# Kernel optimization log

Hardware: AMD Instinct MI355X
Metric: run time of the kernel (lower is better)

## Reference

```python
import jax, jax.numpy as jnp
import numpy as np

B, S, H = 1, 2048, 4096
NH = 32
HD = H // NH  # 128
HALF = HD // 2
BASE = 10000.0


def setup_inputs() -> dict:
    key = jax.random.key(0)
    k1, k2, k3 = jax.random.split(key, 3)
    hidden_states = jax.random.normal(k1, (B, S, H), dtype=jnp.float32)
    W_qkv = jax.random.normal(k2, (H, 3 * H), dtype=jnp.float32) * 0.02
    W_o = jax.random.normal(k3, (H, H), dtype=jnp.float32) * 0.02
    # causal additive mask [B,1,S,S]: 0 on/below diagonal, large negative above
    causal = jnp.triu(jnp.full((S, S), -1e9, dtype=jnp.float32), k=1)
    attention_mask = jnp.broadcast_to(causal[None, None], (B, 1, S, S))
    position_ids = jnp.broadcast_to(jnp.arange(S, dtype=jnp.int64)[None, :], (B, S))
    return {
        'hidden_states': hidden_states,
        'W_qkv': W_qkv,
        'W_o': W_o,
        'attention_mask': attention_mask,
        'position_ids': position_ids,
    }


def _rope(x, cos, sin):
    # x: [b,s,nh,hd]; cos/sin: [b,s,1,half]. Half-split rotation as in the Triton kernel.
    x1, x2 = x[..., :HALF], x[..., HALF:]
    return jnp.concatenate([x1 * cos - x2 * sin, x1 * sin + x2 * cos], axis=-1)


def reference(hidden_states, W_qkv, W_o, attention_mask, position_ids):
    b, s, h = hidden_states.shape
    # fused QKV projection (dequantized GPTQ matmul == dense matmul math)
    qkv = jnp.einsum('bsh,hk->bsk', hidden_states, W_qkv).reshape(b, s, 3, NH, HD)
    # RoPE angles: freq = exp(col * INV_BASE) * position_id, INV_BASE = -2 ln(base)/head_dim
    inv_base = -2.0 * np.log(BASE) / HD
    freqs = jnp.exp(jnp.arange(HALF, dtype=jnp.float32) * inv_base)  # [half]
    theta = position_ids.astype(jnp.float32)[:, :, None] * freqs      # [b,s,half]
    cos = jnp.cos(theta)[:, :, None, :]
    sin = jnp.sin(theta)[:, :, None, :]
    q = _rope(qkv[:, :, 0], cos, sin).transpose(0, 2, 1, 3)  # [b,nh,s,hd]
    k = _rope(qkv[:, :, 1], cos, sin).transpose(0, 2, 1, 3)
    v = qkv[:, :, 2].transpose(0, 2, 1, 3)
    scores = jnp.einsum('bhqd,bhkd->bhqk', q, k) / np.sqrt(HD).astype(np.float32)
    scores = scores + attention_mask
    scores = jnp.maximum(scores, jnp.finfo(scores.dtype).min)
    attn = jax.nn.softmax(scores.astype(jnp.float32), axis=-1).astype(q.dtype)
    out = jnp.einsum('bhqk,bhkd->bqhd', attn, v).reshape(b, s, h)
    return jnp.einsum('bsh,ho->bso', out, W_o)
```

## Files before the change

kernel.cpp:

```cpp
#include <hip/hip_runtime.h>

#define S_LEN 2048
#define HDIM 4096
#define NHEADS 32
#define HEAD_DIM 128
#define HALF_DIM 64
#define N_QKV 12288
#define QK_COLS 8192

typedef __attribute__((ext_vector_type(8))) short short8;
typedef __attribute__((ext_vector_type(4))) float f32x4;

typedef const __attribute__((address_space(1))) unsigned int gu32;
typedef __attribute__((address_space(3))) unsigned int lu32;

__device__ __forceinline__ void gload_lds16(const void* g, void* l) {
    __builtin_amdgcn_global_load_lds((gu32*)g, (lu32*)l, 16, 0, 0);
}

__device__ __forceinline__ unsigned short f2bf(float f) {
    unsigned int u = __float_as_uint(f);
    u += 0x7fff + ((u >> 16) & 1);
    return (unsigned short)(u >> 16);
}

__device__ __forceinline__ void xcd_map(int& bx, int& by) {
    int gx = gridDim.x;
    int lin = blockIdx.y * gx + blockIdx.x;
    int x = lin & 7, c = lin >> 3;
    int bxp = gx >> 3;
    bx = bxp * x + c % bxp;
    by = c / bxp;
}


__global__ __launch_bounds__(256) void cvt_hs_k(const float* __restrict__ in,
                                                unsigned short* __restrict__ out, int n4) {
    int i = blockIdx.x * 256 + threadIdx.x;
    if (i >= n4) return;
    float4 v = reinterpret_cast<const float4*>(in)[i];
    ushort4 o;
    o.x = f2bf(v.x); o.y = f2bf(v.y); o.z = f2bf(v.z); o.w = f2bf(v.w);
    reinterpret_cast<ushort4*>(out)[i] = o;
}

__device__ __forceinline__ int permute_col(int n) {
    if (n < QK_COLS) {
        int hd = n & 127;
        int base = n - hd;
        int e = hd & 63;
        int d2 = (e & 15) + 32 * (e >> 4) + ((hd >> 6) << 4);
        return base + d2;
    }
    return n;
}

template <bool PERM>
__global__ __launch_bounds__(256) void tconv_k(const float* __restrict__ in,
                                               unsigned short* __restrict__ out, int R, int C) {
    __shared__ float tile[64][65];
    int c0 = blockIdx.x * 64, r0 = blockIdx.y * 64;
    int tx = threadIdx.x & 63, ty = threadIdx.x >> 6;
#pragma unroll
    for (int i = 0; i < 16; ++i) {
        int r = ty + i * 4;
        tile[r][tx] = in[(size_t)(r0 + r) * C + c0 + tx];
    }
    __syncthreads();
#pragma unroll
    for (int i = 0; i < 16; ++i) {
        int c = ty + i * 4;
        int n = PERM ? permute_col(c0 + c) : (c0 + c);
        out[(size_t)n * R + r0 + tx] = f2bf(tile[tx][c]);
    }
}

__global__ __launch_bounds__(256) void rope_tab_k(const int* __restrict__ pos_raw,
                                                  float* __restrict__ ctab,
                                                  float* __restrict__ stab) {
    int i = blockIdx.x * 256 + threadIdx.x;
    int s = i >> 6, d = i & 63;
    bool is64 = (pos_raw[1] == 0 && pos_raw[2] == 1);
    int p = is64 ? pos_raw[2 * s] : pos_raw[s];
    const float INVB = -0.14391156831212787f;
    float freq = expf((float)d * INVB);
    float th = (float)p * freq;
    ctab[i] = cosf(th);
    stab[i] = sinf(th);
}


__device__ __forceinline__ void mainloop(const unsigned short* __restrict__ Ag,
                                         const unsigned short* __restrict__ Bg,
                                         int K, int m0, int n0,
                                         char* As, char* Bs,
                                         f32x4 (&acc)[4][4]) {
    const int tid = threadIdx.x;
    const int wid = tid >> 6, lane = tid & 63, l15 = lane & 15, l4 = lane >> 4;
    const int wm = wid >> 1, wn = wid & 1;
    const int NT = K >> 6;

    size_t abase[4], bbase[4];
    int off[4];
#pragma unroll
    for (int i = 0; i < 4; ++i) {
        int p = (i * 256 + tid) << 4;
        int q = p ^ (((p >> 7) & 7) << 4);
        abase[i] = (size_t)(m0 + (q >> 7)) * K + ((q & 127) >> 1);
        bbase[i] = (size_t)(n0 + (q >> 7)) * K + ((q & 127) >> 1);
        off[i] = p;
    }

    for (int t = 0; t < NT; ++t) {
        int k0 = t << 6;
#pragma unroll
        for (int i = 0; i < 4; ++i) gload_lds16(Ag + abase[i] + k0, As + off[i]);
#pragma unroll
        for (int i = 0; i < 4; ++i) gload_lds16(Bg + bbase[i] + k0, Bs + off[i]);
        asm volatile("s_waitcnt vmcnt(0)" ::: "memory");
        __builtin_amdgcn_s_barrier();

        short8 a[4][2], b[4][2];
#pragma unroll
        for (int am = 0; am < 4; ++am)
#pragma unroll
            for (int ks = 0; ks < 2; ++ks) {
                int lin = ((wm * 64 + am * 16 + l15) << 7) + ks * 64 + l4 * 16;
                a[am][ks] = *(const short8*)(As + (lin ^ (((lin >> 7) & 7) << 4)));
            }
#pragma unroll
        for (int bn = 0; bn < 4; ++bn)
#pragma unroll
            for (int ks = 0; ks < 2; ++ks) {
                int lin = ((wn * 64 + bn * 16 + l15) << 7) + ks * 64 + l4 * 16;
                b[bn][ks] = *(const short8*)(Bs + (lin ^ (((lin >> 7) & 7) << 4)));
            }
#pragma unroll
        for (int ks = 0; ks < 2; ++ks)
#pragma unroll
            for (int am = 0; am < 4; ++am)
#pragma unroll
                for (int bn = 0; bn < 4; ++bn)
                    acc[am][bn] = __builtin_amdgcn_mfma_f32_16x16x32_bf16(a[am][ks], b[bn][ks], acc[am][bn], 0, 0, 0);

        __builtin_amdgcn_s_barrier();
    }
}

__global__ __launch_bounds__(256, 3) void gemm1_k(const unsigned short* __restrict__ A,
                                                  const unsigned short* __restrict__ Bt,
                                                  const float* __restrict__ ctab,
                                                  const float* __restrict__ stab,
                                                  unsigned short* __restrict__ qb,
                                                  unsigned short* __restrict__ kb,
                                                  unsigned short* __restrict__ vt) {
    __shared__ __attribute__((aligned(16))) char As[16384];
    __shared__ __attribute__((aligned(16))) char Bs[16384];

    int bx, by;
    xcd_map(bx, by);
    int m0 = by * 128, n0 = bx * 128;

    f32x4 acc[4][4];
#pragma unroll
    for (int i = 0; i < 4; ++i)
#pragma unroll
        for (int j = 0; j < 4; ++j) acc[i][j] = (f32x4){0.f, 0.f, 0.f, 0.f};

    mainloop(A, Bt, HDIM, m0, n0, As, Bs, acc);

    int tid = threadIdx.x, wid = tid >> 6, lane = tid & 63, l15 = lane & 15, l4 = lane >> 4;
    int wm = wid >> 1, wn = wid & 1;
    int which = n0 >> 12;
    int head = (n0 & 4095) >> 7;
    if (which < 2) {
        unsigned short* dst = which ? kb : qb;
#pragma unroll
        for (int am = 0; am < 4; ++am)
#pragma unroll
            for (int j = 0; j < 4; ++j) {
                int s = m0 + wm * 64 + am * 16 + l4 * 4 + j;
#pragma unroll
                for (int p = 0; p < 2; ++p) {
                    float x1 = acc[am][2 * p][j], x2 = acc[am][2 * p + 1][j];
                    int e = l15 + 16 * (2 * wn + p);
                    float cs = ctab[s * 64 + e], sn = stab[s * 64 + e];
                    dst[((size_t)head * S_LEN + s) * HEAD_DIM + e] = f2bf(x1 * cs - x2 * sn);
                    dst[((size_t)head * S_LEN + s) * HEAD_DIM + e + 64] = f2bf(x1 * sn + x2 * cs);
                }
            }
    } else {
#pragma unroll
        for (int am = 0; am < 4; ++am)
#pragma unroll
            for (int j = 0; j < 4; ++j) {
                int s = m0 + wm * 64 + am * 16 + l4 * 4 + j;
#pragma unroll
                for (int bn = 0; bn < 4; ++bn) {
                    int d = wn * 64 + bn * 16 + l15;
                    vt[((size_t)head * HEAD_DIM + d) * S_LEN + s] = f2bf(acc[am][bn][j]);
                }
            }
    }
}

__global__ __launch_bounds__(256, 3) void gemm2_k(const unsigned short* __restrict__ A,
                                                  const unsigned short* __restrict__ Bt,
                                                  float* __restrict__ out) {
    __shared__ __attribute__((aligned(16))) char As[16384];
    __shared__ __attribute__((aligned(16))) char Bs[16384];

    int bx, by;
    xcd_map(bx, by);
    int m0 = by * 128, n0 = bx * 128;

    f32x4 acc[4][4];
#pragma unroll
    for (int i = 0; i < 4; ++i)
#pragma unroll
        for (int j = 0; j < 4; ++j) acc[i][j] = (f32x4){0.f, 0.f, 0.f, 0.f};

    mainloop(A, Bt, HDIM, m0, n0, As, Bs, acc);

    int tid = threadIdx.x, wid = tid >> 6, lane = tid & 63, l15 = lane & 15, l4 = lane >> 4;
    int wm = wid >> 1, wn = wid & 1;
#pragma unroll
    for (int am = 0; am < 4; ++am)
#pragma unroll
        for (int j = 0; j < 4; ++j) {
            int s = m0 + wm * 64 + am * 16 + l4 * 4 + j;
#pragma unroll
            for (int bn = 0; bn < 4; ++bn)
                out[(size_t)s * HDIM + n0 + wn * 64 + bn * 16 + l15] = acc[am][bn][j];
        }
}

__global__ __launch_bounds__(256) void flash_k(const unsigned short* __restrict__ Q,
                                               const unsigned short* __restrict__ Kb,
                                               const unsigned short* __restrict__ Vt,
                                               float* __restrict__ O_parts,
                                               float* __restrict__ ml) {
    __shared__ __attribute__((aligned(16))) char Ks[2][16384];
    __shared__ __attribute__((aligned(16))) char Vs[2][16384];
    __shared__ __attribute__((aligned(16))) char Ps[4][4096];
    int h = blockIdx.y;
    int bx2 = 39 - (int)blockIdx.x;
    int qblk, spl;
    if (bx2 < 4)       { qblk = bx2;                 spl = 0; }
    else if (bx2 < 12) { qblk = 4 + ((bx2 - 4) >> 1);  spl = (bx2 - 4) & 1; }
    else if (bx2 < 24) { int u = bx2 - 12; int q3 = u / 3; qblk = 8 + q3; spl = u - 3 * q3; }
    else               { qblk = 12 + ((bx2 - 24) >> 2); spl = (bx2 - 24) & 3; }
    int pidx = h * 40 + bx2;
    int kv_start = spl << 9;
    int kv_end = min((qblk + 1) << 7, (spl + 1) << 9);
    int NT = (kv_end - kv_start) >> 6;

    int tid = threadIdx.x, w = tid >> 6, lane = tid & 63, l15 = lane & 15, l4 = lane >> 4;
    int qrow0 = qblk * 128 + w * 32;

    const unsigned short* Kg = Kb + (size_t)h * S_LEN * HEAD_DIM;
    const unsigned short* Vg = Vt + (size_t)h * HEAD_DIM * S_LEN;

    short8 qf[2][4];
#pragma unroll
    for (int mt = 0; mt < 2; ++mt) {
        int s = qrow0 + mt * 16 + l15;
#pragma unroll
        for (int ks = 0; ks < 4; ++ks)
            qf[mt][ks] = *(const short8*)(Q + ((size_t)h * S_LEN + s) * HEAD_DIM + ks * 32 + l4 * 8);
    }

    float m_run[2][4];
    f32x4 o[2][8];
    f32x4 lsum[2];
#pragma unroll
    for (int mt = 0; mt < 2; ++mt) {
#pragma unroll
        for (int j = 0; j < 4; ++j) m_run[mt][j] = -1e30f;
        lsum[mt] = (f32x4){0.f, 0.f, 0.f, 0.f};
#pragma unroll
        for (int dt = 0; dt < 8; ++dt) o[mt][dt] = (f32x4){0.f, 0.f, 0.f, 0.f};
    }

    int lofs[4];
    size_t kgofs[4], vgofs[4];
#pragma unroll
    for (int i = 0; i < 4; ++i) {
        int p = (i * 256 + tid) << 4;
        lofs[i] = p;
        int qk = p ^ (((p >> 8) & 7) << 4);
        kgofs[i] = (size_t)(qk >> 8) * HEAD_DIM + ((qk & 255) >> 1);
        int qv = p ^ (((p >> 7) & 7) << 4);
        vgofs[i] = (size_t)(qv >> 7) * S_LEN + ((qv & 127) >> 1);
    }

    auto stage = [&](int t) {
        char* Kd = Ks[t & 1];
        char* Vd = Vs[t & 1];
        size_t kvoff = (size_t)(kv_start + t * 64);
#pragma unroll
        for (int i = 0; i < 4; ++i) gload_lds16(Kg + kvoff * HEAD_DIM + kgofs[i], Kd + lofs[i]);
#pragma unroll
        for (int i = 0; i < 4; ++i) gload_lds16(Vg + kvoff + vgofs[i], Vd + lofs[i]);
    };

    const float scale = 0.08838834764831845f;

    short8 onesv;
#pragma unroll
    for (int e = 0; e < 8; ++e) onesv[e] = (short)0x3F80;

    stage(0);

    for (int t = 0; t < NT; ++t) {
        int cur = t & 1;
        if (t + 1 < NT) {
            stage(t + 1);
            asm volatile("s_waitcnt vmcnt(8)" ::: "memory");
        } else {
            asm volatile("s_waitcnt vmcnt(0)" ::: "memory");
        }
        __builtin_amdgcn_sched_barrier(0);
        __builtin_amdgcn_s_barrier();
        __builtin_amdgcn_sched_barrier(0);

        f32x4 sc[2][4];
#pragma unroll
        for (int mt = 0; mt < 2; ++mt)
#pragma unroll
            for (int nt = 0; nt < 4; ++nt) sc[mt][nt] = (f32x4){0.f, 0.f, 0.f, 0.f};
#pragma unroll
        for (int ks = 0; ks < 4; ++ks) {
            short8 kfr[4];
#pragma unroll
            for (int nt = 0; nt < 4; ++nt) {
                int lin = ((nt * 16 + l15) << 8) + ks * 64 + l4 * 16;
                kfr[nt] = *(const short8*)(Ks[cur] + (lin ^ (((lin >> 8) & 7) << 4)));
            }
#pragma unroll
            for (int mt = 0; mt < 2; ++mt)
#pragma unroll
                for (int nt = 0; nt < 4; ++nt)
                    sc[mt][nt] = __builtin_amdgcn_mfma_f32_16x16x32_bf16(qf[mt][ks], kfr[nt], sc[mt][nt], 0, 0, 0);
        }

        float pmax[2][4];
        bool need = false;
#pragma unroll
        for (int mt = 0; mt < 2; ++mt)
#pragma unroll
            for (int j = 0; j < 4; ++j) {
                int srow = qrow0 + mt * 16 + l4 * 4 + j;
                int c = kv_start + t * 64 + l15;
                float v0 = (c      <= srow) ? sc[mt][0][j] * scale : -1e30f;
                float v1 = (c + 16 <= srow) ? sc[mt][1][j] * scale : -1e30f;
                float v2 = (c + 32 <= srow) ? sc[mt][2][j] * scale : -1e30f;
                float v3 = (c + 48 <= srow) ? sc[mt][3][j] * scale : -1e30f;
                sc[mt][0][j] = v0; sc[mt][1][j] = v1; sc[mt][2][j] = v2; sc[mt][3][j] = v3;
                float mx = fmaxf(fmaxf(v0, v1), fmaxf(v2, v3));
                mx = fmaxf(mx, __shfl_xor(mx, 1));
                mx = fmaxf(mx, __shfl_xor(mx, 2));
                mx = fmaxf(mx, __shfl_xor(mx, 4));
                mx = fmaxf(mx, __shfl_xor(mx, 8));
                pmax[mt][j] = mx;
                need = need || (mx > m_run[mt][j] + 8.0f);
            }
        if (__any(need ? 1 : 0)) {
#pragma unroll
            for (int mt = 0; mt < 2; ++mt)
#pragma unroll
                for (int j = 0; j < 4; ++j) {
                    float mnew = fmaxf(m_run[mt][j], pmax[mt][j]);
                    float r = __expf(m_run[mt][j] - mnew);
                    m_run[mt][j] = mnew;
                    lsum[mt][j] *= r;
#pragma unroll
                    for (int dt = 0; dt < 8; ++dt) o[mt][dt][j] *= r;
                }
        }

#pragma unroll
        for (int mt = 0; mt < 2; ++mt)
#pragma unroll
            for (int j = 0; j < 4; ++j) {
                int prow = mt * 16 + l4 * 4 + j;
                int rb = prow << 7;
                int sw = (prow & 7) << 4;
#pragma unroll
                for (int nt = 0; nt < 4; ++nt) {
                    unsigned short pb = f2bf(__expf(sc[mt][nt][j] - m_run[mt][j]));
                    *(unsigned short*)(Ps[w] + ((rb + (l15 + nt * 16) * 2) ^ sw)) = pb;
                }
            }
        asm volatile("s_waitcnt lgkmcnt(0)" ::: "memory");
        __builtin_amdgcn_sched_barrier(0);

        short8 pf[2][2];
#pragma unroll
        for (int mt = 0; mt < 2; ++mt)
#pragma unroll
            for (int k2 = 0; k2 < 2; ++k2) {
                int lin = ((mt * 16 + l15) << 7) + k2 * 64 + l4 * 16;
                pf[mt][k2] = *(const short8*)(Ps[w] + (lin ^ (((lin >> 7) & 7) << 4)));
            }
#pragma unroll
        for (int k2 = 0; k2 < 2; ++k2)
#pragma unroll
            for (int mt = 0; mt < 2; ++mt)
                lsum[mt] = __builtin_amdgcn_mfma_f32_16x16x32_bf16(pf[mt][k2], onesv, lsum[mt], 0, 0, 0);
#pragma unroll
        for (int dt = 0; dt < 8; ++dt) {
#pragma unroll
            for (int k2 = 0; k2 < 2; ++k2) {
                int lin = ((dt * 16 + l15) << 7) + k2 * 64 + l4 * 16;
                short8 vf = *(const short8*)(Vs[cur] + (lin ^ (((lin >> 7) & 7) << 4)));
#pragma unroll
                for (int mt = 0; mt < 2; ++mt)
                    o[mt][dt] = __builtin_amdgcn_mfma_f32_16x16x32_bf16(pf[mt][k2], vf, o[mt][dt], 0, 0, 0);
            }
        }
        __builtin_amdgcn_sched_barrier(0);
        __builtin_amdgcn_s_barrier();
        __builtin_amdgcn_sched_barrier(0);
    }

    float* Op = O_parts + (size_t)pidx * 16384;
#pragma unroll
    for (int mt = 0; mt < 2; ++mt)
#pragma unroll
        for (int j = 0; j < 4; ++j) {
            int rloc = w * 32 + mt * 16 + l4 * 4 + j;
#pragma unroll
            for (int dt = 0; dt < 8; ++dt)
                Op[rloc * 128 + dt * 16 + l15] = o[mt][dt][j];
            if (l15 == 0) {
                ml[(size_t)pidx * 256 + rloc] = m_run[mt][j];
                ml[(size_t)pidx * 256 + 128 + rloc] = lsum[mt][j];
            }
        }
}

__global__ __launch_bounds__(256) void reduce_k(const float* __restrict__ Op,
                                                const float* __restrict__ ml,
                                                unsigned short* __restrict__ ctx) {
    int qblk = blockIdx.x, h = blockIdx.y;
    int ns = (qblk >> 2) + 1;
    int st;
    if (qblk < 4) st = qblk;
    else if (qblk < 8) st = 4 + 2 * (qblk - 4);
    else if (qblk < 12) st = 12 + 3 * (qblk - 8);
    else st = 24 + 4 * (qblk - 12);
    int p0 = h * 40 + st;
#pragma unroll
    for (int it = 0; it < 16; ++it) {
        int idx = it * 256 + threadIdx.x;
        int row = idx >> 5, dq = idx & 31;
        float mstar = -1e30f;
        for (int s = 0; s < ns; ++s)
            mstar = fmaxf(mstar, ml[(size_t)(p0 + s) * 256 + row]);
        f32x4 acc = (f32x4){0.f, 0.f, 0.f, 0.f};
        float lt = 0.f;
        for (int s = 0; s < ns; ++s) {
            float wgt = __expf(ml[(size_t)(p0 + s) * 256 + row] - mstar);
            lt += wgt * ml[(size_t)(p0 + s) * 256 + 128 + row];
            f32x4 ov = *(const f32x4*)(Op + (size_t)(p0 + s) * 16384 + row * 128 + dq * 4);
            acc += ov * wgt;
        }
        float inv = 1.0f / lt;
        int grow = qblk * 128 + row;
        ushort4 o4;
        o4.x = f2bf(acc[0] * inv);
        o4.y = f2bf(acc[1] * inv);
        o4.z = f2bf(acc[2] * inv);
        o4.w = f2bf(acc[3] * inv);
        *(ushort4*)(ctx + (size_t)grow * HDIM + h * 128 + dq * 4) = o4;
    }
}


extern "C" void kernel_launch(void* const* d_in, const int* in_sizes, int n_in,
                              void* d_out, int out_size, void* d_ws, size_t ws_size,
                              hipStream_t stream) {
    const float* hs = (const float*)d_in[0];
    const float* wqkv = (const float*)d_in[1];
    const float* wo = (const float*)d_in[2];
    const int* pos = (const int*)d_in[4];
    float* out = (float*)d_out;
    char* ws = (char*)d_ws;
    const size_t MB = 1024 * 1024;

    unsigned short* hs_b = (unsigned short*)(ws);
    unsigned short* wq_t = (unsigned short*)(ws + 16 * MB);
    unsigned short* wo_t = (unsigned short*)(ws + 112 * MB);
    unsigned short* qbuf = (unsigned short*)(ws + 144 * MB);
    unsigned short* kbuf = (unsigned short*)(ws + 160 * MB);
    unsigned short* vtb  = (unsigned short*)(ws + 176 * MB);
    unsigned short* ctx  = (unsigned short*)(ws + 192 * MB);
    float* ctab = (float*)(ws + 208 * MB);
    float* stab = (float*)(ws + 209 * MB);
    float* O_parts = (float*)(ws + 16 * MB);
    float* ml_buf  = (float*)(ws + 96 * MB);

    cvt_hs_k<<<(S_LEN * HDIM / 4 + 255) / 256, 256, 0, stream>>>(hs, hs_b, S_LEN * HDIM / 4);
    tconv_k<true><<<dim3(N_QKV / 64, HDIM / 64), 256, 0, stream>>>(wqkv, wq_t, HDIM, N_QKV);
    tconv_k<false><<<dim3(HDIM / 64, HDIM / 64), 256, 0, stream>>>(wo, wo_t, HDIM, HDIM);
    rope_tab_k<<<(S_LEN * 64) / 256, 256, 0, stream>>>(pos, ctab, stab);
    gemm1_k<<<dim3(N_QKV / 128, S_LEN / 128), 256, 0, stream>>>(hs_b, wq_t, ctab, stab, qbuf, kbuf, vtb);
    flash_k<<<dim3(40, NHEADS), 256, 0, stream>>>(qbuf, kbuf, vtb, O_parts, ml_buf);
    reduce_k<<<dim3(S_LEN / 128, NHEADS), 256, 0, stream>>>(O_parts, ml_buf, ctx);
    gemm2_k<<<dim3(HDIM / 128, S_LEN / 128), 256, 0, stream>>>(ctx, wo_t, out);
}
```

Before: 541.1 us.

## Fold softmax scale into Q RoPE, store bf16 partials, raise MFMA priority

Folds the 1/sqrt(head_dim) scale into the RoPE cos/sin factors for Q in the QKV GEMM epilogue, which removes the per-score multiply in the flash kernel. Stores the split-KV partial outputs as bf16 instead of fp32, halving the partial-output write and read traffic between flash_k and reduce_k at some cost in precision. Also wraps the MFMA loops in s_setprio so MFMA-issuing waves get scheduling priority.

```diff
diff --git a/kernel.cpp b/kernel.cpp
--- a/kernel.cpp
+++ b/kernel.cpp
@@ -22,6 +22,10 @@
     unsigned int u = __float_as_uint(f);
     u += 0x7fff + ((u >> 16) & 1);
     return (unsigned short)(u >> 16);
+}
+
+__device__ __forceinline__ float bf2f(unsigned short b) {
+    return __uint_as_float((unsigned int)b << 16);
 }
 
 __device__ __forceinline__ void xcd_map(int& bx, int& by) {
@@ -175,6 +179,7 @@
     int head = (n0 & 4095) >> 7;
     if (which < 2) {
         unsigned short* dst = which ? kb : qb;
+        float qs = which ? 1.0f : 0.08838834764831845f;
 #pragma unroll
         for (int am = 0; am < 4; ++am)
 #pragma unroll
@@ -184,7 +189,7 @@
                 for (int p = 0; p < 2; ++p) {
                     float x1 = acc[am][2 * p][j], x2 = acc[am][2 * p + 1][j];
                     int e = l15 + 16 * (2 * wn + p);
-                    float cs = ctab[s * 64 + e], sn = stab[s * 64 + e];
+                    float cs = ctab[s * 64 + e] * qs, sn = stab[s * 64 + e] * qs;
                     dst[((size_t)head * S_LEN + s) * HEAD_DIM + e] = f2bf(x1 * cs - x2 * sn);
                     dst[((size_t)head * S_LEN + s) * HEAD_DIM + e + 64] = f2bf(x1 * sn + x2 * cs);
                 }
@@ -238,7 +243,7 @@
 __global__ __launch_bounds__(256) void flash_k(const unsigned short* __restrict__ Q,
                                                const unsigned short* __restrict__ Kb,
                                                const unsigned short* __restrict__ Vt,
-                                               float* __restrict__ O_parts,
+                                               unsigned short* __restrict__ O_parts,
                                                float* __restrict__ ml) {
     __shared__ __attribute__((aligned(16))) char Ks[2][16384];
     __shared__ __attribute__((aligned(16))) char Vs[2][16384];
@@ -304,8 +309,6 @@
         for (int i = 0; i < 4; ++i) gload_lds16(Vg + kvoff + vgofs[i], Vd + lofs[i]);
     };
 
-    const float scale = 0.08838834764831845f;
-
     short8 onesv;
 #pragma unroll
     for (int e = 0; e < 8; ++e) onesv[e] = (short)0x3F80;
@@ -329,6 +332,7 @@
         for (int mt = 0; mt < 2; ++mt)
 #pragma unroll
             for (int nt = 0; nt < 4; ++nt) sc[mt][nt] = (f32x4){0.f, 0.f, 0.f, 0.f};
+        __builtin_amdgcn_s_setprio(1);
 #pragma unroll
         for (int ks = 0; ks < 4; ++ks) {
             short8 kfr[4];
@@ -343,6 +347,7 @@
                 for (int nt = 0; nt < 4; ++nt)
                     sc[mt][nt] = __builtin_amdgcn_mfma_f32_16x16x32_bf16(qf[mt][ks], kfr[nt], sc[mt][nt], 0, 0, 0);
         }
+        __builtin_amdgcn_s_setprio(0);
 
         float pmax[2][4];
         bool need = false;
@@ -352,10 +357,10 @@
             for (int j = 0; j < 4; ++j) {
                 int srow = qrow0 + mt * 16 + l4 * 4 + j;
                 int c = kv_start + t * 64 + l15;
-                float v0 = (c      <= srow) ? sc[mt][0][j] * scale : -1e30f;
-                float v1 = (c + 16 <= srow) ? sc[mt][1][j] * scale : -1e30f;
-                float v2 = (c + 32 <= srow) ? sc[mt][2][j] * scale : -1e30f;
-                float v3 = (c + 48 <= srow) ? sc[mt][3][j] * scale : -1e30f;
+                float v0 = (c      <= srow) ? sc[mt][0][j] : -1e30f;
+                float v1 = (c + 16 <= srow) ? sc[mt][1][j] : -1e30f;
+                float v2 = (c + 32 <= srow) ? sc[mt][2][j] : -1e30f;
+                float v3 = (c + 48 <= srow) ? sc[mt][3][j] : -1e30f;
                 sc[mt][0][j] = v0; sc[mt][1][j] = v1; sc[mt][2][j] = v2; sc[mt][3][j] = v3;
                 float mx = fmaxf(fmaxf(v0, v1), fmaxf(v2, v3));
                 mx = fmaxf(mx, __shfl_xor(mx, 1));
@@ -403,6 +408,7 @@
                 int lin = ((mt * 16 + l15) << 7) + k2 * 64 + l4 * 16;
                 pf[mt][k2] = *(const short8*)(Ps[w] + (lin ^ (((lin >> 7) & 7) << 4)));
             }
+        __builtin_amdgcn_s_setprio(1);
 #pragma unroll
         for (int k2 = 0; k2 < 2; ++k2)
 #pragma unroll
@@ -419,12 +425,13 @@
                     o[mt][dt] = __builtin_amdgcn_mfma_f32_16x16x32_bf16(pf[mt][k2], vf, o[mt][dt], 0, 0, 0);
             }
         }
+        __builtin_amdgcn_s_setprio(0);
         __builtin_amdgcn_sched_barrier(0);
         __builtin_amdgcn_s_barrier();
         __builtin_amdgcn_sched_barrier(0);
     }
 
-    float* Op = O_parts + (size_t)pidx * 16384;
+    unsigned short* Op = O_parts + (size_t)pidx * 16384;
 #pragma unroll
     for (int mt = 0; mt < 2; ++mt)
 #pragma unroll
@@ -432,7 +439,7 @@
             int rloc = w * 32 + mt * 16 + l4 * 4 + j;
 #pragma unroll
             for (int dt = 0; dt < 8; ++dt)
-                Op[rloc * 128 + dt * 16 + l15] = o[mt][dt][j];
+                Op[rloc * 128 + dt * 16 + l15] = f2bf(o[mt][dt][j]);
             if (l15 == 0) {
                 ml[(size_t)pidx * 256 + rloc] = m_run[mt][j];
                 ml[(size_t)pidx * 256 + 128 + rloc] = lsum[mt][j];
@@ -440,7 +447,7 @@
         }
 }
 
-__global__ __launch_bounds__(256) void reduce_k(const float* __restrict__ Op,
+__global__ __launch_bounds__(256) void reduce_k(const unsigned short* __restrict__ Op,
                                                 const float* __restrict__ ml,
                                                 unsigned short* __restrict__ ctx) {
     int qblk = blockIdx.x, h = blockIdx.y;
@@ -463,8 +470,11 @@
         for (int s = 0; s < ns; ++s) {
             float wgt = __expf(ml[(size_t)(p0 + s) * 256 + row] - mstar);
             lt += wgt * ml[(size_t)(p0 + s) * 256 + 128 + row];
-            f32x4 ov = *(const f32x4*)(Op + (size_t)(p0 + s) * 16384 + row * 128 + dq * 4);
-            acc += ov * wgt;
+            ushort4 ov = *(const ushort4*)(Op + (size_t)(p0 + s) * 16384 + row * 128 + dq * 4);
+            acc[0] += bf2f(ov.x) * wgt;
+            acc[1] += bf2f(ov.y) * wgt;
+            acc[2] += bf2f(ov.z) * wgt;
+            acc[3] += bf2f(ov.w) * wgt;
         }
         float inv = 1.0f / lt;
         int grow = qblk * 128 + row;
@@ -498,8 +508,8 @@
     unsigned short* ctx  = (unsigned short*)(ws + 192 * MB);
     float* ctab = (float*)(ws + 208 * MB);
     float* stab = (float*)(ws + 209 * MB);
-    float* O_parts = (float*)(ws + 16 * MB);
-    float* ml_buf  = (float*)(ws + 96 * MB);
+    unsigned short* O_parts = (unsigned short*)(ws + 16 * MB);
+    float* ml_buf = (float*)(ws + 96 * MB);
 
     cvt_hs_k<<<(S_LEN * HDIM / 4 + 255) / 256, 256, 0, stream>>>(hs, hs_b, S_LEN * HDIM / 4);
     tconv_k<true><<<dim3(N_QKV / 64, HDIM / 64), 256, 0, stream>>>(wqkv, wq_t, HDIM, N_QKV);
```

Result: no change. 533.7 us, median of 2 (-1.4%).
